# Kernel tuning notes

Hardware: AMD Instinct MI355X
Metric: run time of the kernel (lower is better)

Reference implementation:

```python
import jax, jax.numpy as jnp
import numpy as np

EPS = 1e-6
NEG = -1e9

def rotate_half(x):
    x1, x2 = jnp.split(x, 2, axis=-1)
    return jnp.concatenate([-x2, x1], axis=-1)

def setup_inputs() -> dict:
    key = jax.random.key(0)
    ks = jax.random.split(key, 5)
    T, d_model, n_h = 2048, 2048, 16
    d_h = d_model // n_h
    x = jax.random.normal(ks[0], (T, d_model), dtype=jnp.float32)
    # RoPE tables (realistic rotary angles)
    inv_freq = 1.0 / (10000.0 ** (jnp.arange(0, d_h, 2, dtype=jnp.float32) / d_h))
    t = jnp.arange(T, dtype=jnp.float32)
    freqs = jnp.einsum('t,f->tf', t, inv_freq)
    emb = jnp.concatenate([freqs, freqs], axis=-1)  # [T, d_h]
    cos, sin = jnp.cos(emb), jnp.sin(emb)
    attention_mask = jnp.ones((T,), dtype=bool)
    ln_w = jnp.ones((d_model,), dtype=jnp.float32)
    w_qkv = jax.random.normal(ks[1], (3 * d_model, d_model), dtype=jnp.float32) / np.sqrt(d_model)
    w_o = jax.random.normal(ks[2], (d_model, d_model), dtype=jnp.float32) / np.sqrt(d_model)
    return {"x": x, "cos": cos, "sin": sin, "attention_mask": attention_mask,
            "ln_w": ln_w, "w_qkv": w_qkv, "w_o": w_o}

def reference(x, cos, sin, attention_mask, ln_w, w_qkv, w_o):
    T, d_model = x.shape
    n_h = 16
    d_h = d_model // n_h
    scale = 1.0 / np.sqrt(d_h)
    # RMSNorm
    ms = jnp.mean(x * x, axis=-1, keepdims=True)
    h = ln_w * x * jax.lax.rsqrt(ms + EPS)
    # fused QKV projection (eqx Linear: y = W @ x => h @ W.T)
    qkv = (h @ w_qkv.T).reshape(T, 3, n_h, d_h)
    q = qkv[:, 0].transpose(1, 0, 2)  # [H, T, d_h]
    k = qkv[:, 1].transpose(1, 0, 2)
    v = qkv[:, 2].transpose(1, 0, 2)
    # RoPE (cos/sin broadcast over heads)
    q = q * cos + rotate_half(q) * sin
    k = k * cos + rotate_half(k) * sin
    # attention scores with causal + padding mask
    scores = jnp.einsum('hqd,hkd->hqk', q, k) * scale
    causal = jnp.tril(jnp.ones((T, T), dtype=bool))[None]
    am = attention_mask.astype(bool)
    valid = causal & am[None, None, :]
    scores = jnp.where(valid, scores, NEG)
    scores = jnp.where(am[None, :, None], scores, NEG)
    probs = jax.nn.softmax(scores, axis=-1)
    out = jnp.einsum('hqk,hkd->hqd', probs, v)  # [H, T, d_h]
    out = out.transpose(1, 0, 2).reshape(T, d_model)
    out = out @ w_o.T
    out = jnp.where(attention_mask[:, None], out, 0.0)
    return x + out
```

## Files before the change

kernel.cpp:

```cpp
#include <hip/hip_runtime.h>


#define T_SEQ 2048
#define DM 2048
#define NH 16
#define DH 128
#define DM3 6144

typedef short s16x8 __attribute__((ext_vector_type(8)));
typedef float f32x4 __attribute__((ext_vector_type(4)));

static __device__ __forceinline__ unsigned short f2bf(float f){
  unsigned u = __builtin_bit_cast(unsigned, f);
  u += 0x7FFFu + ((u>>16)&1u);
  return (unsigned short)(u>>16);
}
static __device__ __forceinline__ float bf2f(unsigned short b){
  return __builtin_bit_cast(float, ((unsigned)b)<<16);
}
static __device__ __forceinline__ void gload_lds16(const void* g, void* l){
  __builtin_amdgcn_global_load_lds((const __attribute__((address_space(1))) void*)g,
                                   (__attribute__((address_space(3))) void*)l, 16, 0, 0);
}

__global__ __launch_bounds__(256) void cast_kernel(const float4* __restrict__ wq,
                                                   const float4* __restrict__ wo,
                                                   ushort4* __restrict__ wqo,
                                                   ushort4* __restrict__ woo,
                                                   int nq4, int ntot4){
  int i = blockIdx.x*256 + threadIdx.x;
  if (i >= ntot4) return;
  float4 v;
  if (i < nq4) v = wq[i]; else v = wo[i - nq4];
  ushort4 o; o.x=f2bf(v.x); o.y=f2bf(v.y); o.z=f2bf(v.z); o.w=f2bf(v.w);
  if (i < nq4) wqo[i] = o; else woo[i - nq4] = o;
}

__global__ __launch_bounds__(256) void rmsnorm_kernel(const float* __restrict__ x,
                                                      const float* __restrict__ w,
                                                      unsigned short* __restrict__ h){
  int row = blockIdx.x;
  int tid = threadIdx.x;
  const float4* xr = (const float4*)(x + (size_t)row*DM);
  float4 v0 = xr[tid], v1 = xr[tid+256];
  float ss = v0.x*v0.x+v0.y*v0.y+v0.z*v0.z+v0.w*v0.w
           + v1.x*v1.x+v1.y*v1.y+v1.z*v1.z+v1.w*v1.w;
  #pragma unroll
  for (int off=32; off; off>>=1) ss += __shfl_xor(ss, off, 64);
  __shared__ float wsum[4];
  if ((tid&63)==0) wsum[tid>>6] = ss;
  __syncthreads();
  float rs = rsqrtf((wsum[0]+wsum[1]+wsum[2]+wsum[3]) * (1.0f/DM) + 1e-6f);
  const float4* w4 = (const float4*)w;
  float4 wa = w4[tid], wb = w4[tid+256];
  ushort4* h4 = (ushort4*)(h + (size_t)row*DM);
  ushort4 o0, o1;
  o0.x=f2bf(v0.x*wa.x*rs); o0.y=f2bf(v0.y*wa.y*rs); o0.z=f2bf(v0.z*wa.z*rs); o0.w=f2bf(v0.w*wa.w*rs);
  o1.x=f2bf(v1.x*wb.x*rs); o1.y=f2bf(v1.y*wb.y*rs); o1.z=f2bf(v1.z*wb.z*rs); o1.w=f2bf(v1.w*wb.w*rs);
  h4[tid] = o0; h4[tid+256] = o1;
}

template <typename OUTT>
__global__ __launch_bounds__(256) void gemm_bt(const unsigned short* __restrict__ A,
                                               const unsigned short* __restrict__ B,
                                               OUTT* __restrict__ C,
                                               const float* __restrict__ resid,
                                               int M, int N, int K){
  __shared__ __align__(16) unsigned short As[128*32];
  __shared__ __align__(16) unsigned short Bs[128*32];
  int tid = threadIdx.x, lane = tid&63, wid = tid>>6;
  int c16 = lane&15, g = lane>>4;
  int bm = blockIdx.y, bn = blockIdx.x;
  int wr = wid>>1, wc = wid&1;
  f32x4 acc[4][4] = {};
  int nk = K >> 5;
  const char* Ab = (const char*)A;
  const char* Bb = (const char*)B;
  for (int ko=0; ko<nk; ++ko){
    #pragma unroll
    for (int c=0;c<2;c++){
      int li = (wid*2+c)*1024 + lane*16;
      int row = li>>6, colb = li&63;
      gload_lds16(Ab + ((size_t)(bm*128+row)*K + ko*32)*2 + colb,
                  (char*)As + (wid*2+c)*1024);
      gload_lds16(Bb + ((size_t)(bn*128+row)*K + ko*32)*2 + colb,
                  (char*)Bs + (wid*2+c)*1024);
    }
    __syncthreads();
    s16x8 af[4], bfr[4];
    #pragma unroll
    for (int m=0;m<4;m++) af[m]  = *(const s16x8*)&As[(wr*64+m*16+c16)*32 + g*8];
    #pragma unroll
    for (int n=0;n<4;n++) bfr[n] = *(const s16x8*)&Bs[(wc*64+n*16+c16)*32 + g*8];
    #pragma unroll
    for (int m=0;m<4;m++)
      #pragma unroll
      for (int n=0;n<4;n++)
        acc[m][n] = __builtin_amdgcn_mfma_f32_16x16x32_bf16(af[m], bfr[n], acc[m][n], 0,0,0);
    __syncthreads();
  }
  #pragma unroll
  for (int m=0;m<4;m++)
    #pragma unroll
    for (int n=0;n<4;n++){
      int r0 = bm*128 + wr*64 + m*16 + g*4;
      int c0 = bn*128 + wc*64 + n*16 + c16;
      #pragma unroll
      for (int r=0;r<4;r++){
        float v = acc[m][n][r];
        if (resid) v += resid[(size_t)(r0+r)*N + c0];
        if constexpr (__is_same(OUTT, float))
          C[(size_t)(r0+r)*N + c0] = v;
        else
          C[(size_t)(r0+r)*N + c0] = f2bf(v);
      }
    }
}

__global__ __launch_bounds__(256) void rope_kernel(const unsigned short* __restrict__ qkv,
                                                   const float* __restrict__ cs,
                                                   const float* __restrict__ sn,
                                                   unsigned short* __restrict__ Qr,
                                                   unsigned short* __restrict__ Kr){
  int idx = blockIdx.x*256 + threadIdx.x;
  int dh = idx & 63;
  int h  = (idx>>6) & (NH-1);
  int t  = idx >> 10;
  size_t base = (size_t)t*DM3 + h*DH;
  float c = cs[t*DH + dh], s = sn[t*DH + dh];
  float q1 = bf2f(qkv[base+dh]),      q2 = bf2f(qkv[base+dh+64]);
  float k1 = bf2f(qkv[base+DM+dh]),   k2 = bf2f(qkv[base+DM+dh+64]);
  const float sc = 0.088388347648318447f;
  size_t ob = ((size_t)h*T_SEQ + t)*DH + dh;
  Qr[ob]    = f2bf((q1*c - q2*s)*sc);
  Qr[ob+64] = f2bf((q2*c + q1*s)*sc);
  Kr[ob]    = f2bf(k1*c - k2*s);
  Kr[ob+64] = f2bf(k2*c + k1*s);
}

__global__ __launch_bounds__(256) void vtrans_kernel(const unsigned short* __restrict__ qkv,
                                                     unsigned short* __restrict__ Vt){
  __shared__ unsigned short tile[32][33];
  int t0 = blockIdx.x*32, d0 = blockIdx.y*32, h = blockIdx.z;
  int c = threadIdx.x & 31, r0 = threadIdx.x >> 5;
  #pragma unroll
  for (int i=0;i<4;i++){
    int r = r0 + i*8;
    tile[r][c] = qkv[(size_t)(t0+r)*DM3 + 2*DM + h*DH + d0 + c];
  }
  __syncthreads();
  #pragma unroll
  for (int i=0;i<4;i++){
    int d = r0 + i*8;
    Vt[((size_t)h*DH + d0 + d)*T_SEQ + t0 + c] = tile[c][d];
  }
}

__global__ __launch_bounds__(256) void attn_kernel(const unsigned short* __restrict__ Qr,
                                                   const unsigned short* __restrict__ Kr,
                                                   const unsigned short* __restrict__ Vt,
                                                   unsigned short* __restrict__ O){
  __shared__ __align__(16) unsigned short Plds[4][16][40];
  __shared__ float sm[4][16];
  __shared__ float sl[4][16];
  __shared__ __align__(16) unsigned short so[4][16][128];
  int tid = threadIdx.x;
  int lane = tid & 63, wid = tid >> 6;
  int c16 = lane & 15, g = lane >> 4;
  int id = blockIdx.x;
  int h  = id & 15;
  int qt = 127 - (id >> 4);
  int qr0 = qt * 16;
  const unsigned short* Qh = Qr + (size_t)h*T_SEQ*DH;
  const unsigned short* Kh = Kr + (size_t)h*T_SEQ*DH;
  const unsigned short* Vh = Vt + (size_t)h*DH*T_SEQ;
  s16x8 aq[4];
  #pragma unroll
  for (int kk=0;kk<4;kk++)
    aq[kk] = *(const s16x8*)&Qh[(size_t)(qr0+c16)*DH + kk*32 + g*8];
  f32x4 o[8] = {};
  float m[4] = {-1e30f,-1e30f,-1e30f,-1e30f};
  float l[4] = {0.f,0.f,0.f,0.f};
  int nkv = (qr0 + 47) >> 5;
  int it0 = (wid*nkv) >> 2, it1 = ((wid+1)*nkv) >> 2;
  for (int it = it0; it < it1; ++it){
    int kv0 = it * 32;
    f32x4 sf[2] = {};
    #pragma unroll
    for (int n=0;n<2;n++)
      #pragma unroll
      for (int kk=0;kk<4;kk++){
        s16x8 bk = *(const s16x8*)&Kh[(size_t)(kv0+n*16+c16)*DH + kk*32 + g*8];
        sf[n] = __builtin_amdgcn_mfma_f32_16x16x32_bf16(aq[kk], bk, sf[n], 0,0,0);
      }
    if (kv0 + 31 > qr0){
      #pragma unroll
      for (int n=0;n<2;n++)
        #pragma unroll
        for (int r=0;r<4;r++)
          if (kv0+n*16+c16 > qr0+g*4+r) sf[n][r] = -1e30f;
    }
    float sc[4];
    #pragma unroll
    for (int r=0;r<4;r++){
      float mx = fmaxf(sf[0][r], sf[1][r]);
      #pragma unroll
      for (int off=1; off<16; off<<=1) mx = fmaxf(mx, __shfl_xor(mx, off, 16));
      float mnew = fmaxf(m[r], mx);
      sc[r] = __expf(m[r] - mnew);
      m[r] = mnew;
      float p0 = __expf(sf[0][r]-mnew), p1 = __expf(sf[1][r]-mnew);
      sf[0][r]=p0; sf[1][r]=p1;
      float rsum = p0+p1;
      #pragma unroll
      for (int off=1; off<16; off<<=1) rsum += __shfl_xor(rsum, off, 16);
      l[r] = l[r]*sc[r] + rsum;
    }
    #pragma unroll
    for (int n2=0;n2<8;n2++)
      #pragma unroll
      for (int r=0;r<4;r++) o[n2][r] *= sc[r];
    #pragma unroll
    for (int n=0;n<2;n++)
      #pragma unroll
      for (int r=0;r<4;r++)
        Plds[wid][g*4+r][n*16+c16] = f2bf(sf[n][r]);
    s16x8 pa = *(const s16x8*)&Plds[wid][c16][g*8];
    #pragma unroll
    for (int n2=0;n2<8;n2++){
      s16x8 bv = *(const s16x8*)&Vh[(size_t)(n2*16+c16)*T_SEQ + kv0 + g*8];
      o[n2] = __builtin_amdgcn_mfma_f32_16x16x32_bf16(pa, bv, o[n2], 0,0,0);
    }
  }
  if (c16 == 0){
    #pragma unroll
    for (int r=0;r<4;r++){ sm[wid][g*4+r] = m[r]; sl[wid][g*4+r] = l[r]; }
  }
  #pragma unroll
  for (int n2=0;n2<8;n2++)
    #pragma unroll
    for (int r=0;r<4;r++)
      so[wid][g*4+r][n2*16+c16] = f2bf(o[n2][r]);
  __syncthreads();
  int row = tid >> 4;
  int col = (tid & 15) * 8;
  float mg = fmaxf(fmaxf(sm[0][row], sm[1][row]), fmaxf(sm[2][row], sm[3][row]));
  float lg = 0.f;
  float acc[8] = {};
  #pragma unroll
  for (int w=0;w<4;w++){
    float e = __expf(sm[w][row] - mg);
    lg += sl[w][row] * e;
    #pragma unroll
    for (int j=0;j<8;j++) acc[j] += e * bf2f(so[w][row][col+j]);
  }
  float inv = 1.0f / lg;
  s16x8 ov;
  #pragma unroll
  for (int j=0;j<8;j++) ov[j] = (short)f2bf(acc[j]*inv);
  *(s16x8*)&O[(size_t)(qr0+row)*DM + h*DH + col] = ov;
}

extern "C" void kernel_launch(void* const* d_in, const int* in_sizes, int n_in,
                              void* d_out, int out_size, void* d_ws, size_t ws_size,
                              hipStream_t stream){
  const float* x    = (const float*)d_in[0];
  const float* cs   = (const float*)d_in[1];
  const float* sn   = (const float*)d_in[2];
  const float* ln_w = (const float*)d_in[4];
  const float* wqkv = (const float*)d_in[5];
  const float* wo   = (const float*)d_in[6];

  char* ws = (char*)d_ws;
  unsigned short* h     = (unsigned short*)(ws);
  unsigned short* wqkvb = (unsigned short*)(ws + 8388608);
  unsigned short* wob   = (unsigned short*)(ws + 33554432);
  unsigned short* qkv   = (unsigned short*)(ws + 41943040);
  unsigned short* attno = qkv;
  unsigned short* Qr    = (unsigned short*)(ws + 67108864);
  unsigned short* Kr    = (unsigned short*)(ws + 75497472);
  unsigned short* Vt    = (unsigned short*)(ws + 83886080);
  float* out            = (float*)d_out;

  cast_kernel<<<16384, 256, 0, stream>>>((const float4*)wqkv, (const float4*)wo,
                                         (ushort4*)wqkvb, (ushort4*)wob,
                                         3145728, 4194304);
  rmsnorm_kernel<<<2048, 256, 0, stream>>>(x, ln_w, h);
  gemm_bt<unsigned short><<<dim3(48,16), 256, 0, stream>>>(h, wqkvb, qkv, nullptr, 2048, 6144, 2048);
  rope_kernel<<<8192, 256, 0, stream>>>(qkv, cs, sn, Qr, Kr);
  vtrans_kernel<<<dim3(64,4,16), 256, 0, stream>>>(qkv, Vt);
  attn_kernel<<<dim3(2048), 256, 0, stream>>>(Qr, Kr, Vt, attno);
  gemm_bt<float><<<dim3(16,16), 256, 0, stream>>>(attno, wob, out, x, 2048, 2048, 2048);
}
```

Baseline: 398.6 us.

## Compute transposed S tile to keep P in registers, dropping LDS round-trip

The QK^T MFMA now swaps its operands and uses a permuted K row mapping. Each lane then holds eight scores for a single query column, so after the 16-lane group reduction the exp values can be packed straight into the A operand of the PV MFMA. This removes the per-iteration LDS store and reload of P and the 16-wide shuffle reductions, which drop to two shuffles per reduction. It adds a broadcast shuffle of the rescale factor, and correctness depends on the permuted key ordering lining up with V's k-index layout.

```diff
diff --git a/kernel.cpp b/kernel.cpp
--- a/kernel.cpp
+++ b/kernel.cpp
@@ -17,6 +17,9 @@
 }
 static __device__ __forceinline__ float bf2f(unsigned short b){
   return __builtin_bit_cast(float, ((unsigned)b)<<16);
+}
+static __device__ __forceinline__ unsigned pk2bf(float a, float b){
+  return (unsigned)f2bf(a) | ((unsigned)f2bf(b) << 16);
 }
 static __device__ __forceinline__ void gload_lds16(const void* g, void* l){
   __builtin_amdgcn_global_load_lds((const __attribute__((address_space(1))) void*)g,
@@ -160,7 +163,6 @@
                                                    const unsigned short* __restrict__ Kr,
                                                    const unsigned short* __restrict__ Vt,
                                                    unsigned short* __restrict__ O){
-  __shared__ __align__(16) unsigned short Plds[4][16][40];
   __shared__ float sm[4][16];
   __shared__ float sl[4][16];
   __shared__ __align__(16) unsigned short so[4][16][128];
@@ -179,8 +181,8 @@
   for (int kk=0;kk<4;kk++)
     aq[kk] = *(const s16x8*)&Qh[(size_t)(qr0+c16)*DH + kk*32 + g*8];
   f32x4 o[8] = {};
-  float m[4] = {-1e30f,-1e30f,-1e30f,-1e30f};
-  float l[4] = {0.f,0.f,0.f,0.f};
+  float m_q = -1e30f, l_q = 0.f;
+  int sig = 8*(c16>>2) + (c16&3);
   int nkv = (qr0 + 47) >> 5;
   int it0 = (wid*nkv) >> 2, it1 = ((wid+1)*nkv) >> 2;
   for (int it = it0; it < it1; ++it){
@@ -190,52 +192,49 @@
     for (int n=0;n<2;n++)
       #pragma unroll
       for (int kk=0;kk<4;kk++){
-        s16x8 bk = *(const s16x8*)&Kh[(size_t)(kv0+n*16+c16)*DH + kk*32 + g*8];
-        sf[n] = __builtin_amdgcn_mfma_f32_16x16x32_bf16(aq[kk], bk, sf[n], 0,0,0);
+        s16x8 bk = *(const s16x8*)&Kh[(size_t)(kv0 + sig + 4*n)*DH + kk*32 + g*8];
+        sf[n] = __builtin_amdgcn_mfma_f32_16x16x32_bf16(bk, aq[kk], sf[n], 0,0,0);
       }
     if (kv0 + 31 > qr0){
       #pragma unroll
       for (int n=0;n<2;n++)
         #pragma unroll
         for (int r=0;r<4;r++)
-          if (kv0+n*16+c16 > qr0+g*4+r) sf[n][r] = -1e30f;
-    }
-    float sc[4];
-    #pragma unroll
-    for (int r=0;r<4;r++){
-      float mx = fmaxf(sf[0][r], sf[1][r]);
-      #pragma unroll
-      for (int off=1; off<16; off<<=1) mx = fmaxf(mx, __shfl_xor(mx, off, 16));
-      float mnew = fmaxf(m[r], mx);
-      sc[r] = __expf(m[r] - mnew);
-      m[r] = mnew;
-      float p0 = __expf(sf[0][r]-mnew), p1 = __expf(sf[1][r]-mnew);
-      sf[0][r]=p0; sf[1][r]=p1;
-      float rsum = p0+p1;
-      #pragma unroll
-      for (int off=1; off<16; off<<=1) rsum += __shfl_xor(rsum, off, 16);
-      l[r] = l[r]*sc[r] + rsum;
-    }
+          if (kv0 + 8*g + 4*n + r > qr0 + c16) sf[n][r] = -1e30f;
+    }
+    float mx = fmaxf(fmaxf(fmaxf(sf[0][0],sf[0][1]), fmaxf(sf[0][2],sf[0][3])),
+                     fmaxf(fmaxf(sf[1][0],sf[1][1]), fmaxf(sf[1][2],sf[1][3])));
+    mx = fmaxf(mx, __shfl_xor(mx, 16));
+    mx = fmaxf(mx, __shfl_xor(mx, 32));
+    float mnew = fmaxf(m_q, mx);
+    float sc = __expf(m_q - mnew);
+    m_q = mnew;
+    float p[8];
+    #pragma unroll
+    for (int n=0;n<2;n++)
+      #pragma unroll
+      for (int r=0;r<4;r++) p[4*n+r] = __expf(sf[n][r] - mnew);
+    float rs = ((p[0]+p[1])+(p[2]+p[3])) + ((p[4]+p[5])+(p[6]+p[7]));
+    rs += __shfl_xor(rs, 16);
+    rs += __shfl_xor(rs, 32);
+    l_q = l_q*sc + rs;
+    union { unsigned u[4]; s16x8 v; } pau;
+    pau.u[0] = pk2bf(p[0],p[1]); pau.u[1] = pk2bf(p[2],p[3]);
+    pau.u[2] = pk2bf(p[4],p[5]); pau.u[3] = pk2bf(p[6],p[7]);
+    float scr[4];
+    #pragma unroll
+    for (int r=0;r<4;r++) scr[r] = __shfl(sc, g*4 + r);
     #pragma unroll
     for (int n2=0;n2<8;n2++)
       #pragma unroll
-      for (int r=0;r<4;r++) o[n2][r] *= sc[r];
-    #pragma unroll
-    for (int n=0;n<2;n++)
-      #pragma unroll
-      for (int r=0;r<4;r++)
-        Plds[wid][g*4+r][n*16+c16] = f2bf(sf[n][r]);
-    s16x8 pa = *(const s16x8*)&Plds[wid][c16][g*8];
+      for (int r=0;r<4;r++) o[n2][r] *= scr[r];
     #pragma unroll
     for (int n2=0;n2<8;n2++){
       s16x8 bv = *(const s16x8*)&Vh[(size_t)(n2*16+c16)*T_SEQ + kv0 + g*8];
-      o[n2] = __builtin_amdgcn_mfma_f32_16x16x32_bf16(pa, bv, o[n2], 0,0,0);
-    }
-  }
-  if (c16 == 0){
-    #pragma unroll
-    for (int r=0;r<4;r++){ sm[wid][g*4+r] = m[r]; sl[wid][g*4+r] = l[r]; }
-  }
+      o[n2] = __builtin_amdgcn_mfma_f32_16x16x32_bf16(pau.v, bv, o[n2], 0,0,0);
+    }
+  }
+  if (lane < 16){ sm[wid][lane] = m_q; sl[wid][lane] = l_q; }
   #pragma unroll
   for (int n2=0;n2<8;n2++)
     #pragma unroll
```

Result: faster. 390.1 us (-2.1%).
